# Performance work log

Measured on AMD Instinct MI355X. Metric: run time of the kernel, lower is better.

## Reference

```python
import jax, jax.numpy as jnp
import numpy as np


def setup_inputs() -> dict:
    key = jax.random.key(0)
    k1, k2, k3 = jax.random.split(key, 3)
    B, Cin, H, W = 64, 16, 256, 256
    Cout, K = 64, 3
    x = jax.random.normal(k1, (B, Cin, H, W), dtype=jnp.float32)
    # PyTorch Conv2d init scale ~ 1/sqrt(fan_in)
    fan_in = Cin * K * K
    conv_weight = jax.random.normal(k2, (Cout, Cin, K, K), dtype=jnp.float32) / np.sqrt(fan_in)
    conv_bias = jax.random.normal(k3, (Cout,), dtype=jnp.float32) / np.sqrt(fan_in)
    return {"x": x, "conv_weight": conv_weight, "conv_bias": conv_bias}


def reference(x, conv_weight, conv_bias):
    # Conv2d: stride=1, padding=0 (VALID), dilation=1, groups=1
    y = jax.lax.conv_general_dilated(
        x, conv_weight,
        window_strides=(1, 1),
        padding="VALID",
        dimension_numbers=("NCHW", "OIHW", "NCHW"),
    ) + conv_bias[None, :, None, None]          # [B, Cout, 254, 254]
    m = jnp.min(y, axis=1, keepdims=True)        # [B, 1, 254, 254] min over channels
    return jnp.tanh(jnp.tanh(m))                 # double tanh
```

## Files before the change

### kernel.cpp

```cpp
#include <hip/hip_runtime.h>
#include <math.h>

#define CIN    16
#define COUT   64
#define H      256
#define W      256
#define OH     254
#define OW     254
#define NTAP   9
#define RING   10

typedef _Float16 f16x8  __attribute__((ext_vector_type(8)));
typedef float    f32x16 __attribute__((ext_vector_type(16)));

#define XSLOT(w, g) ((((w) << 1) | (g)) ^ (((w) >> 2) & 7))

__global__ void wpack_kernel(const float* __restrict__ w, _Float16* __restrict__ wpk) {
    int idx = blockIdx.x * 256 + threadIdx.x;
    if (idx >= NTAP * 2 * 64 * 8) return;
    int e = idx & 7, l = (idx >> 3) & 63, m = (idx >> 9) & 1, t = idx >> 10;
    int co  = (l & 31) + 32 * m;
    int cin = 8 * (l >> 5) + e;
    wpk[idx] = (_Float16)w[((co * CIN + cin) * 3 + t / 3) * 3 + (t % 3)];
}

__device__ __forceinline__ float tanh_fast(float v) {
    float e = __expf(2.0f * v);
    return 1.0f - 2.0f * __builtin_amdgcn_rcpf(e + 1.0f);
}

__global__ __launch_bounds__(512, 2) void conv_mfma_kernel(
        const float* __restrict__ x, const f16x8* __restrict__ wpk,
        const float* __restrict__ bias, float* __restrict__ out) {
    __shared__ f16x8 xs[RING * 512 + 64];

    const int tid = threadIdx.x;
    const int b   = blockIdx.x >> 2;
    const int s   = blockIdx.x & 3;
    const int oh0 = s * 64;
    const int npairs = (s == 3) ? 31 : 32;

    const float* xb = x + (size_t)b * CIN * H * W;

    const int lane = tid & 63;
    f16x8 wreg[NTAP][2];
#pragma unroll
    for (int t = 0; t < NTAP; ++t)
#pragma unroll
        for (int m = 0; m < 2; ++m)
            wreg[t][m] = wpk[(t * 2 + m) * 64 + lane];

    const int gld  = tid >> 8;
    const int rld  = (tid >> 7) & 1;
    const int pp   = tid & 127;
    const int w2   = pp * 2;

#define STAGE(rowAbs, slot)                                                     \
    {                                                                           \
        int row_ = (rowAbs) > 255 ? 255 : (rowAbs);                             \
        const float* p_ = xb + (size_t)row_ * W + w2;                           \
        float2 vv_[8];                                                          \
        _Pragma("unroll")                                                       \
        for (int c = 0; c < 8; ++c)                                             \
            vv_[c] = *(const float2*)(p_ + (size_t)(8 * gld + c) * (H * W));    \
        f16x8 q0, q1;                                                           \
        _Pragma("unroll")                                                       \
        for (int c = 0; c < 8; ++c) { q0[c] = (_Float16)vv_[c].x;               \
                                      q1[c] = (_Float16)vv_[c].y; }             \
        xs[(slot) * 512 + XSLOT(w2,     gld)] = q0;                             \
        xs[(slot) * 512 + XSLOT(w2 + 1, gld)] = q1;                             \
    }

#pragma unroll
    for (int i = 0; i < 3; ++i)
        STAGE(oh0 + 2 * i + rld, 2 * i + rld)
    __syncthreads();

    const int wave = tid >> 6;
    const int ohl  = wave >> 2;
    const int ph   = (wave & 3) * 64;
    const int l31  = lane & 31;
    const int g2   = lane >> 5;

    int off[3][2];
#pragma unroll
    for (int kw = 0; kw < 3; ++kw)
#pragma unroll
        for (int n = 0; n < 2; ++n) {
            int w = ph + 32 * n + l31 + kw;
            if (w > 255) w = 255;
            off[kw][n] = XSLOT(w, g2);
        }

    float binit[2][16];
#pragma unroll
    for (int m = 0; m < 2; ++m)
#pragma unroll
        for (int r = 0; r < 16; ++r)
            binit[m][r] = bias[(r & 3) + 8 * (r >> 2) + 4 * g2 + 32 * m];

    f32x16 acc[2][2];
#pragma unroll
    for (int m = 0; m < 2; ++m)
#pragma unroll
        for (int n = 0; n < 2; ++n)
#pragma unroll
            for (int r = 0; r < 16; ++r)
                acc[m][n][r] = binit[m][r];

    for (int p = 0; p < npairs; ++p) {
        int ldrow = oh0 + 2 * p + 6 + rld;
        if (ldrow > 255) ldrow = 255;
        const float* lp = xb + (size_t)ldrow * W + w2;
        float2 vv[8];
#pragma unroll
        for (int c = 0; c < 8; ++c)
            vv[c] = *(const float2*)(lp + (size_t)(8 * gld + c) * (H * W));

        const int hb = 2 * p + ohl;
        const f16x8* xr0 = xs + (hb % RING) * 512;
        const f16x8* xr1 = xs + ((hb + 1) % RING) * 512;
        const f16x8* xr2 = xs + ((hb + 2) % RING) * 512;

#pragma unroll
        for (int t = 0; t < NTAP; ++t) {
            const int kh = t / 3, kw = t % 3;
            const f16x8* xr = (kh == 0) ? xr0 : (kh == 1) ? xr1 : xr2;
#pragma unroll
            for (int n = 0; n < 2; ++n) {
                f16x8 bf = xr[off[kw][n]];
                acc[0][n] = __builtin_amdgcn_mfma_f32_32x32x16_f16(wreg[t][0], bf, acc[0][n], 0, 0, 0);
                acc[1][n] = __builtin_amdgcn_mfma_f32_32x32x16_f16(wreg[t][1], bf, acc[1][n], 0, 0, 0);
            }
        }

        const int oh = oh0 + 2 * p + ohl;
#pragma unroll
        for (int n = 0; n < 2; ++n) {
            float mn = fminf(acc[0][n][0], acc[1][n][0]);
#pragma unroll
            for (int r = 1; r < 16; ++r)
                mn = fminf(mn, fminf(acc[0][n][r], acc[1][n][r]));
            mn = fminf(mn, __shfl_xor(mn, 32));
            float t2 = tanh_fast(tanh_fast(mn));
            int px = ph + 32 * n + l31;
            if (g2 == 0 && px < OW)
                out[((size_t)b * OH + oh) * OW + px] = t2;
#pragma unroll
            for (int m = 0; m < 2; ++m)
#pragma unroll
                for (int r = 0; r < 16; ++r)
                    acc[m][n][r] = binit[m][r];
        }

        {
            const int slot = (2 * p + 6 + rld) % RING;
            f16x8 q0, q1;
#pragma unroll
            for (int c = 0; c < 8; ++c) { q0[c] = (_Float16)vv[c].x;
                                          q1[c] = (_Float16)vv[c].y; }
            xs[slot * 512 + XSLOT(w2,     gld)] = q0;
            xs[slot * 512 + XSLOT(w2 + 1, gld)] = q1;
        }

        if (p & 1) __syncthreads();
    }
}

extern "C" void kernel_launch(void* const* d_in, const int* in_sizes, int n_in,
                              void* d_out, int out_size, void* d_ws, size_t ws_size,
                              hipStream_t stream) {
    const float* x    = (const float*)d_in[0];
    const float* w    = (const float*)d_in[1];
    const float* bias = (const float*)d_in[2];
    float* out = (float*)d_out;
    _Float16* wpk = (_Float16*)d_ws;

    wpack_kernel<<<36, 256, 0, stream>>>(w, wpk);
    conv_mfma_kernel<<<64 * 4, 512, 0, stream>>>(x, (const f16x8*)wpk, bias, out);
}
```

Baseline: 93.43 us.

## Split conv into 32-row strips with 256-thread blocks and one row per iteration

Blocks now cover 32 output rows with 4 waves each handling one row at a time, instead of 64-row strips with 8 waves handling row pairs. The grid doubles to 512 blocks, the LDS ring shrinks to 6 slots, and staging loads now fetch one float per channel per thread. Bias is folded into the first MFMA's accumulator input instead of reinitialising the accumulators after each row. The aim is more blocks to fill the CUs and less register pressure. The cost is that halo rows are re-read more often and the per-thread loads are narrower scalar loads instead of float2 loads.

```diff
diff --git a/kernel.cpp b/kernel.cpp
--- a/kernel.cpp
+++ b/kernel.cpp
@@ -8,7 +8,8 @@
 #define OH     254
 #define OW     254
 #define NTAP   9
-#define RING   10
+#define RING   6
+#define STRIP  32
 
 typedef _Float16 f16x8  __attribute__((ext_vector_type(8)));
 typedef float    f32x16 __attribute__((ext_vector_type(16)));
@@ -29,20 +30,19 @@
     return 1.0f - 2.0f * __builtin_amdgcn_rcpf(e + 1.0f);
 }
 
-__global__ __launch_bounds__(512, 2) void conv_mfma_kernel(
+__global__ __launch_bounds__(256, 2) void conv_mfma_kernel(
         const float* __restrict__ x, const f16x8* __restrict__ wpk,
         const float* __restrict__ bias, float* __restrict__ out) {
-    __shared__ f16x8 xs[RING * 512 + 64];
+    __shared__ f16x8 xs[RING * 512];
 
     const int tid = threadIdx.x;
-    const int b   = blockIdx.x >> 2;
-    const int s   = blockIdx.x & 3;
-    const int oh0 = s * 64;
-    const int npairs = (s == 3) ? 31 : 32;
+    const int b   = blockIdx.x >> 3;
+    const int s   = blockIdx.x & 7;
+    const int oh0 = s * STRIP;
 
     const float* xb = x + (size_t)b * CIN * H * W;
+    const int lane = tid & 63;
 
-    const int lane = tid & 63;
     f16x8 wreg[NTAP][2];
 #pragma unroll
     for (int t = 0; t < NTAP; ++t)
@@ -50,37 +50,17 @@
         for (int m = 0; m < 2; ++m)
             wreg[t][m] = wpk[(t * 2 + m) * 64 + lane];
 
-    const int gld  = tid >> 8;
-    const int rld  = (tid >> 7) & 1;
-    const int pp   = tid & 127;
-    const int w2   = pp * 2;
-
-#define STAGE(rowAbs, slot)                                                     \
-    {                                                                           \
-        int row_ = (rowAbs) > 255 ? 255 : (rowAbs);                             \
-        const float* p_ = xb + (size_t)row_ * W + w2;                           \
-        float2 vv_[8];                                                          \
-        _Pragma("unroll")                                                       \
-        for (int c = 0; c < 8; ++c)                                             \
-            vv_[c] = *(const float2*)(p_ + (size_t)(8 * gld + c) * (H * W));    \
-        f16x8 q0, q1;                                                           \
-        _Pragma("unroll")                                                       \
-        for (int c = 0; c < 8; ++c) { q0[c] = (_Float16)vv_[c].x;               \
-                                      q1[c] = (_Float16)vv_[c].y; }             \
-        xs[(slot) * 512 + XSLOT(w2,     gld)] = q0;                             \
-        xs[(slot) * 512 + XSLOT(w2 + 1, gld)] = q1;                             \
-    }
-
-#pragma unroll
-    for (int i = 0; i < 3; ++i)
-        STAGE(oh0 + 2 * i + rld, 2 * i + rld)
-    __syncthreads();
-
     const int wave = tid >> 6;
-    const int ohl  = wave >> 2;
-    const int ph   = (wave & 3) * 64;
+    const int ph   = wave * 64;
     const int l31  = lane & 31;
     const int g2   = lane >> 5;
+
+    f32x16 cbias[2];
+#pragma unroll
+    for (int m = 0; m < 2; ++m)
+#pragma unroll
+        for (int r = 0; r < 16; ++r)
+            cbias[m][r] = bias[(r & 3) + 8 * (r >> 2) + 4 * g2 + 32 * m];
 
     int off[3][2];
 #pragma unroll
@@ -92,78 +72,81 @@
             off[kw][n] = XSLOT(w, g2);
         }
 
-    float binit[2][16];
+#define STAGE_LOAD(rowAbs, v)                                                   \
+    {                                                                           \
+        int row_ = (rowAbs) > 255 ? 255 : (rowAbs);                             \
+        const float* p_ = xb + (size_t)row_ * W + tid;                          \
+        _Pragma("unroll")                                                       \
+        for (int c = 0; c < CIN; ++c) v[c] = p_[(size_t)c * (H * W)];           \
+    }
+#define STAGE_WRITE(slot, v)                                                    \
+    {                                                                           \
+        f16x8 q0, q1;                                                           \
+        _Pragma("unroll")                                                       \
+        for (int c = 0; c < 8; ++c) { q0[c] = (_Float16)v[c];                   \
+                                      q1[c] = (_Float16)v[c + 8]; }             \
+        xs[(slot) * 512 + XSLOT(tid, 0)] = q0;                                  \
+        xs[(slot) * 512 + XSLOT(tid, 1)] = q1;                                  \
+    }
+
 #pragma unroll
-    for (int m = 0; m < 2; ++m)
-#pragma unroll
-        for (int r = 0; r < 16; ++r)
-            binit[m][r] = bias[(r & 3) + 8 * (r >> 2) + 4 * g2 + 32 * m];
+    for (int i = 0; i < 4; ++i) {
+        float v[CIN];
+        STAGE_LOAD(oh0 + i, v)
+        STAGE_WRITE(i, v)
+    }
+    __syncthreads();
 
-    f32x16 acc[2][2];
-#pragma unroll
-    for (int m = 0; m < 2; ++m)
-#pragma unroll
-        for (int n = 0; n < 2; ++n)
-#pragma unroll
-            for (int r = 0; r < 16; ++r)
-                acc[m][n][r] = binit[m][r];
+    int rs0 = 0, rs1 = 1, rs2 = 2, wsl = 4;
 
-    for (int p = 0; p < npairs; ++p) {
-        int ldrow = oh0 + 2 * p + 6 + rld;
-        if (ldrow > 255) ldrow = 255;
-        const float* lp = xb + (size_t)ldrow * W + w2;
-        float2 vv[8];
-#pragma unroll
-        for (int c = 0; c < 8; ++c)
-            vv[c] = *(const float2*)(lp + (size_t)(8 * gld + c) * (H * W));
+    for (int r = 0; r < STRIP; ++r) {
+        float v[CIN];
+        STAGE_LOAD(oh0 + r + 4, v)
 
-        const int hb = 2 * p + ohl;
-        const f16x8* xr0 = xs + (hb % RING) * 512;
-        const f16x8* xr1 = xs + ((hb + 1) % RING) * 512;
-        const f16x8* xr2 = xs + ((hb + 2) % RING) * 512;
+        const f16x8* x0 = xs + rs0 * 512;
+        const f16x8* x1 = xs + rs1 * 512;
+        const f16x8* x2 = xs + rs2 * 512;
 
+        f32x16 acc[2][2];
 #pragma unroll
         for (int t = 0; t < NTAP; ++t) {
             const int kh = t / 3, kw = t % 3;
-            const f16x8* xr = (kh == 0) ? xr0 : (kh == 1) ? xr1 : xr2;
+            const f16x8* xr = (kh == 0) ? x0 : (kh == 1) ? x1 : x2;
 #pragma unroll
             for (int n = 0; n < 2; ++n) {
                 f16x8 bf = xr[off[kw][n]];
-                acc[0][n] = __builtin_amdgcn_mfma_f32_32x32x16_f16(wreg[t][0], bf, acc[0][n], 0, 0, 0);
-                acc[1][n] = __builtin_amdgcn_mfma_f32_32x32x16_f16(wreg[t][1], bf, acc[1][n], 0, 0, 0);
+                if (t == 0) {
+                    acc[0][n] = __builtin_amdgcn_mfma_f32_32x32x16_f16(wreg[0][0], bf, cbias[0], 0, 0, 0);
+                    acc[1][n] = __builtin_amdgcn_mfma_f32_32x32x16_f16(wreg[0][1], bf, cbias[1], 0, 0, 0);
+                } else {
+                    acc[0][n] = __builtin_amdgcn_mfma_f32_32x32x16_f16(wreg[t][0], bf, acc[0][n], 0, 0, 0);
+                    acc[1][n] = __builtin_amdgcn_mfma_f32_32x32x16_f16(wreg[t][1], bf, acc[1][n], 0, 0, 0);
+                }
             }
         }
 
-        const int oh = oh0 + 2 * p + ohl;
+        const int oh = oh0 + r;
 #pragma unroll
         for (int n = 0; n < 2; ++n) {
             float mn = fminf(acc[0][n][0], acc[1][n][0]);
 #pragma unroll
-            for (int r = 1; r < 16; ++r)
-                mn = fminf(mn, fminf(acc[0][n][r], acc[1][n][r]));
+            for (int q = 1; q < 16; ++q)
+                mn = fminf(mn, fminf(acc[0][n][q], acc[1][n][q]));
             mn = fminf(mn, __shfl_xor(mn, 32));
             float t2 = tanh_fast(tanh_fast(mn));
             int px = ph + 32 * n + l31;
-            if (g2 == 0 && px < OW)
+            if (g2 == 0 && px < OW && oh < OH)
                 out[((size_t)b * OH + oh) * OW + px] = t2;
-#pragma unroll
-            for (int m = 0; m < 2; ++m)
-#pragma unroll
-                for (int r = 0; r < 16; ++r)
-                    acc[m][n][r] = binit[m][r];
         }
 
-        {
-            const int slot = (2 * p + 6 + rld) % RING;
-            f16x8 q0, q1;
-#pragma unroll
-            for (int c = 0; c < 8; ++c) { q0[c] = (_Float16)vv[c].x;
-                                          q1[c] = (_Float16)vv[c].y; }
-            xs[slot * 512 + XSLOT(w2,     gld)] = q0;
-            xs[slot * 512 + XSLOT(w2 + 1, gld)] = q1;
-        }
+        STAGE_WRITE(wsl, v)
 
-        if (p & 1) __syncthreads();
+        if (r & 1) __syncthreads();
+
+        rs0 = (rs0 == RING - 1) ? 0 : rs0 + 1;
+        rs1 = (rs1 == RING - 1) ? 0 : rs1 + 1;
+        rs2 = (rs2 == RING - 1) ? 0 : rs2 + 1;
+        wsl = (wsl == RING - 1) ? 0 : wsl + 1;
     }
 }
 
@@ -177,5 +160,5 @@
     _Float16* wpk = (_Float16*)d_ws;
 
     wpack_kernel<<<36, 256, 0, stream>>>(w, wpk);
-    conv_mfma_kernel<<<64 * 4, 512, 0, stream>>>(x, (const f16x8*)wpk, bias, out);
+    conv_mfma_kernel<<<64 * 8, 256, 0, stream>>>(x, (const f16x8*)wpk, bias, out);
 }
```

Measured after the change: 94.37 us. No clear change (+1.0%).
